# Kernel optimization log

Hardware: AMD Instinct MI355X
Metric: run time of the kernel (lower is better)

Reference implementation:

```python
import jax, jax.numpy as jnp
import numpy as np


def _conv1x1(x, W, b):
    # x: [B, Cin, H, W]; W: [Cout, Cin]; b: [Cout] -- 1x1 conv == channel matmul
    return jnp.einsum('oc,bchw->bohw', W, x) + b[None, :, None, None]


def setup_inputs() -> dict:
    key = jax.random.key(0)
    ks = jax.random.split(key, 9)
    B, C, H, W = 8, 64, 64, 64
    x = jax.random.normal(ks[0], (B, C, H, W), dtype=jnp.float32)
    y = jax.random.normal(ks[1], (B, C, H, W), dtype=jnp.float32)
    scale = 1.0 / np.sqrt(C)
    Wq = jax.random.normal(ks[2], (C, C), dtype=jnp.float32) * scale
    bq = jax.random.normal(ks[3], (C,), dtype=jnp.float32) * 0.01
    Wk = jax.random.normal(ks[4], (C, C), dtype=jnp.float32) * scale
    bk = jax.random.normal(ks[5], (C,), dtype=jnp.float32) * 0.01
    Wv = jax.random.normal(ks[6], (C, C), dtype=jnp.float32) * scale
    bv = jax.random.normal(ks[7], (C,), dtype=jnp.float32) * 0.01
    # torch inits gamma to 0; use small nonzero value so output/grads are non-trivial
    gamma = jax.random.normal(ks[8], (1,), dtype=jnp.float32) * 0.1
    return {"x": x, "y": y, "Wq": Wq, "bq": bq, "Wk": Wk, "bk": bk,
            "Wv": Wv, "bv": bv, "gamma": gamma}


def reference(x, y, Wq, bq, Wk, bk, Wv, bv, gamma):
    B, C, H, W = x.shape
    N = H * W
    q = _conv1x1(x, Wq, bq)  # [B, C, H, W]
    k = _conv1x1(y, Wk, bk)
    v = _conv1x1(y, Wv, bv)
    # Faithful to torch: raw .view(B, -1, C) memory reinterpretation (NOT a transpose)
    qf = q.reshape(B, N, C)   # reinterprets [B,C,H,W] buffer as [B, N, C]
    kf = k.reshape(B, C, N)
    vf = v.reshape(B, C, N)
    att = jnp.einsum('bnc,bcm->bnm', qf, kf)          # [B, N, N], unscaled
    att = jax.nn.softmax(att, axis=-1)
    out = jnp.einsum('bcj,bij->bci', vf, att)         # bmm(v, att^T) -> [B, C, N]
    out = out.reshape(B, C, H, W)
    return gamma[0] * out + x
```

## Files before the change

### kernel.cpp

```cpp
#include <hip/hip_runtime.h>
#include <math.h>

#define Bb 8
#define Cc 64
#define Nn 4096

typedef __attribute__((ext_vector_type(8))) short bf16x8;
typedef __attribute__((ext_vector_type(4))) float f32x4;
typedef __attribute__((ext_vector_type(4))) int   i32x4;

#define MFMA(a,b,c) __builtin_amdgcn_mfma_f32_16x16x32_bf16((a),(b),(c),0,0,0)

__device__ __forceinline__ unsigned short f2bf(float f){
    unsigned uu = __float_as_uint(f);
    return (unsigned short)((uu + 0x7FFFu + ((uu>>16)&1u)) >> 16);
}
__device__ __forceinline__ int swzaddr(int row, int slot){
    int h = (row ^ (row>>3)) & 7;
    return row*128 + (((slot ^ h)&7)<<4);
}

#define YT0   0
#define YTT0  8192
#define P0    16384

__global__ __launch_bounds__(512, 2) void fused_attn_mfma(
    const float* __restrict__ x, const float* __restrict__ y,
    const float* __restrict__ Wq, const float* __restrict__ bq,
    const float* __restrict__ Wk, const float* __restrict__ bk,
    const float* __restrict__ Wv, const float* __restrict__ bv,
    const float* __restrict__ gammap, float* __restrict__ out)
{
    __shared__ __align__(16) float QbL[2*4096];
    __shared__ __align__(16) unsigned char RBp[32768];
    __shared__ float qbsL[128];
    __shared__ float WqL[128];
    __shared__ float bqL[2];
    __shared__ float bkL[64];

    const int tid = threadIdx.x;
    const int l   = tid & 63;
    const int w   = tid >> 6;
    const int l15 = l & 15;
    const int u   = l >> 4;
    const int b   = blockIdx.x >> 5;
    const int pb  = blockIdx.x & 31;
    const int c0  = pb*2;
    const int p0  = pb*128;

    const float* __restrict__ xb = x + (size_t)b*Cc*Nn;
    const float* __restrict__ yb = y + (size_t)b*Cc*Nn;

    if (tid < 128) WqL[tid] = Wq[c0*64 + tid];
    if (tid < 2)   bqL[tid] = bq[c0 + tid];
    if (tid < 64)  bkL[tid] = bk[tid];
    {
        float* WkL = (float*)RBp;
        #pragma unroll
        for (int q2 = 0; q2 < 2; ++q2){
            const int idx = tid*8 + q2*4;
            *(float4*)(&WkL[idx]) = *(const float4*)(Wk + idx);
        }
    }
    __syncthreads();

    {
        const int pp = tid*8;
        float q0[8], q1[8];
        const float bq0 = bqL[0], bq1 = bqL[1];
        #pragma unroll
        for (int k2=0;k2<8;++k2){ q0[k2]=bq0; q1[k2]=bq1; }
        #pragma unroll 4
        for (int cx=0; cx<64; ++cx){
            const float wa = WqL[cx], wb = WqL[64+cx];
            const float4 x0 = *(const float4*)(xb + cx*Nn + pp);
            const float4 x1 = *(const float4*)(xb + cx*Nn + pp + 4);
            q0[0]=fmaf(wa,x0.x,q0[0]); q0[1]=fmaf(wa,x0.y,q0[1]);
            q0[2]=fmaf(wa,x0.z,q0[2]); q0[3]=fmaf(wa,x0.w,q0[3]);
            q0[4]=fmaf(wa,x1.x,q0[4]); q0[5]=fmaf(wa,x1.y,q0[5]);
            q0[6]=fmaf(wa,x1.z,q0[6]); q0[7]=fmaf(wa,x1.w,q0[7]);
            q1[0]=fmaf(wb,x0.x,q1[0]); q1[1]=fmaf(wb,x0.y,q1[1]);
            q1[2]=fmaf(wb,x0.z,q1[2]); q1[3]=fmaf(wb,x0.w,q1[3]);
            q1[4]=fmaf(wb,x1.x,q1[4]); q1[5]=fmaf(wb,x1.y,q1[5]);
            q1[6]=fmaf(wb,x1.z,q1[6]); q1[7]=fmaf(wb,x1.w,q1[7]);
        }
        *(float4*)(&QbL[pp])        = make_float4(q0[0],q0[1],q0[2],q0[3]);
        *(float4*)(&QbL[pp+4])      = make_float4(q0[4],q0[5],q0[6],q0[7]);
        *(float4*)(&QbL[4096+pp])   = make_float4(q1[0],q1[1],q1[2],q1[3]);
        *(float4*)(&QbL[4096+pp+4]) = make_float4(q1[4],q1[5],q1[6],q1[7]);
    }
    __syncthreads();

    if (tid < 128) {
        const float* qr = &QbL[(tid>>6)*4096 + (tid&63)*64];
        float a = 0.f;
        #pragma unroll 8
        for (int c=0;c<64;++c) a = fmaf(qr[c], bkL[c], a);
        qbsL[tid] = a;
    }
    f32x4 D2[4];
    {
        const float* WkL = (const float*)RBp;
        bf16x8 wkA[4][2];
        #pragma unroll
        for (int mb=0; mb<4; ++mb){
            const int ci = mb*16 + l15;
            #pragma unroll
            for (int kc=0; kc<2; ++kc){
                bf16x8 t;
                #pragma unroll
                for (int i=0;i<8;++i) t[i] = (short)f2bf(WkL[(kc*32 + u*8 + i)*64 + ci]);
                wkA[mb][kc] = t;
            }
        }
        bf16x8 qbB[2];
        {
            const int t = w*16 + l15;
            const float* qr = &QbL[(t>>6)*4096 + (t&63)*64];
            #pragma unroll
            for (int kc=0; kc<2; ++kc){
                const float4 f0 = *(const float4*)(qr + kc*32 + u*8);
                const float4 f1 = *(const float4*)(qr + kc*32 + u*8 + 4);
                bf16x8 t;
                t[0]=(short)f2bf(f0.x); t[1]=(short)f2bf(f0.y);
                t[2]=(short)f2bf(f0.z); t[3]=(short)f2bf(f0.w);
                t[4]=(short)f2bf(f1.x); t[5]=(short)f2bf(f1.y);
                t[6]=(short)f2bf(f1.z); t[7]=(short)f2bf(f1.w);
                qbB[kc] = t;
            }
        }
        #pragma unroll
        for (int mb=0;mb<4;++mb){
            f32x4 d = {0.f,0.f,0.f,0.f};
            d = MFMA(wkA[mb][0], qbB[0], d);
            d = MFMA(wkA[mb][1], qbB[1], d);
            D2[mb] = d;
        }
    }
    __syncthreads();

    unsigned char* QWp = (unsigned char*)QbL;
    {
        const int t = w*16 + l15;
        #pragma unroll
        for (int mb=0;mb<4;++mb){
            #pragma unroll
            for (int r=0;r<4;++r){
                const int ci = mb*16 + u*4 + r;
                *(unsigned short*)(QWp + swzaddr(t, ci>>3) + (ci&7)*2) = f2bf(D2[mb][r]);
            }
        }
    }
    bf16x8 qwA0, qwA1;
    {
        const int t = w*16 + l15;
        qwA0 = *(const bf16x8*)(QWp + swzaddr(t, u));
        qwA1 = *(const bf16x8*)(QWp + swzaddr(t, 4 + u));
    }
    float qb4[4];
    #pragma unroll
    for (int r=0;r<4;++r) qb4[r] = qbsL[w*16 + u*4 + r];

    const int sci = tid >> 3;
    const int sjj = (tid & 7) * 8;
    int rA[4][2], paA[2], pwA2[4][4], trA[8];
    #pragma unroll
    for (int nb=0;nb<4;++nb){
        const int row = 16*nb + l15;
        rA[nb][0] = swzaddr(row, u);
        rA[nb][1] = swzaddr(row, 4 + u);
    }
    paA[0] = P0 + swzaddr(w*16 + l15, u);
    paA[1] = P0 + swzaddr(w*16 + l15, 4 + u);
    #pragma unroll
    for (int r=0;r<4;++r){
        const int trow = w*16 + u*4 + r;
        #pragma unroll
        for (int nb=0;nb<4;++nb)
            pwA2[r][nb] = P0 + swzaddr(trow, (l15>>3) + 2*nb) + (l&7)*2;
    }
    const int natA = YT0 + swzaddr(sci, tid & 7);
    #pragma unroll
    for (int k=0;k<8;++k)
        trA[k] = YTT0 + swzaddr(sjj + k, sci>>3) + (sci&7)*2;

    f32x4 PY[4];
    #pragma unroll
    for (int nb=0;nb<4;++nb) PY[nb] = (f32x4){0.f,0.f,0.f,0.f};
    float m4[4], l4[4];
    #pragma unroll
    for (int r=0;r<4;++r){ m4[r] = -1.0e30f; l4[r] = 0.f; }

    const float* ybt = yb + sci*Nn + sjj;
    float4 ra0 = *(const float4*)(ybt);
    float4 ra1 = *(const float4*)(ybt + 4);
    float4 rb0, rb1;

    auto tile_body = [&](int jt, float4& A0, float4& A1, float4& N0, float4& N1) {
        unsigned short e0=f2bf(A0.x), e1=f2bf(A0.y), e2=f2bf(A0.z), e3=f2bf(A0.w);
        unsigned short e4=f2bf(A1.x), e5=f2bf(A1.y), e6=f2bf(A1.z), e7=f2bf(A1.w);
        i32x4 pk;
        pk.x = (int)e0 | ((int)e1<<16);
        pk.y = (int)e2 | ((int)e3<<16);
        pk.z = (int)e4 | ((int)e5<<16);
        pk.w = (int)e6 | ((int)e7<<16);
        *(i32x4*)(RBp + natA) = pk;
        *(unsigned short*)(RBp + trA[0]) = e0;
        *(unsigned short*)(RBp + trA[1]) = e1;
        *(unsigned short*)(RBp + trA[2]) = e2;
        *(unsigned short*)(RBp + trA[3]) = e3;
        *(unsigned short*)(RBp + trA[4]) = e4;
        *(unsigned short*)(RBp + trA[5]) = e5;
        *(unsigned short*)(RBp + trA[6]) = e6;
        *(unsigned short*)(RBp + trA[7]) = e7;
        __syncthreads();
        {
            const float* yn = ybt + ((jt+1)&63)*64;
            N0 = *(const float4*)(yn);
            N1 = *(const float4*)(yn + 4);
        }
        f32x4 S[4];
        #pragma unroll
        for (int nb=0;nb<4;++nb){
            f32x4 s = (f32x4){qb4[0],qb4[1],qb4[2],qb4[3]};
            s = MFMA(qwA0, *(const bf16x8*)(RBp + YTT0 + rA[nb][0]), s);
            s = MFMA(qwA1, *(const bf16x8*)(RBp + YTT0 + rA[nb][1]), s);
            S[nb] = s;
        }
        float pm[4];
        #pragma unroll
        for (int r=0;r<4;++r)
            pm[r] = fmaxf(fmaxf(S[0][r],S[1][r]), fmaxf(S[2][r],S[3][r]));
        #pragma unroll
        for (int st=1; st<16; st<<=1){
            #pragma unroll
            for (int r=0;r<4;++r) pm[r] = fmaxf(pm[r], __shfl_xor(pm[r], st));
        }
        float sc[4], rs[4];
        #pragma unroll
        for (int r=0;r<4;++r){
            const float mn = fmaxf(m4[r], pm[r]);
            sc[r] = __expf(m4[r] - mn);
            m4[r] = mn;
            rs[r] = 0.f;
        }
        #pragma unroll
        for (int nb=0;nb<4;++nb){
            #pragma unroll
            for (int r=0;r<4;++r){
                const float e = __expf(S[nb][r] - m4[r]);
                S[nb][r] = e;
                rs[r] += e;
            }
        }
        #pragma unroll
        for (int st=1; st<16; st<<=1){
            #pragma unroll
            for (int r=0;r<4;++r) rs[r] += __shfl_xor(rs[r], st);
        }
        #pragma unroll
        for (int r=0;r<4;++r) l4[r] = l4[r]*sc[r] + rs[r];
        #pragma unroll
        for (int nb=0;nb<4;++nb){
            #pragma unroll
            for (int r=0;r<4;++r) PY[nb][r] *= sc[r];
        }
        #pragma unroll
        for (int r=0;r<4;++r){
            #pragma unroll
            for (int nb=0;nb<4;++nb)
                *(unsigned short*)(RBp + pwA2[r][nb]) = f2bf(S[nb][r]);
        }
        bf16x8 pa0 = *(const bf16x8*)(RBp + paA[0]);
        bf16x8 pa1 = *(const bf16x8*)(RBp + paA[1]);
        #pragma unroll
        for (int nb=0;nb<4;++nb){
            f32x4 acc = PY[nb];
            acc = MFMA(pa0, *(const bf16x8*)(RBp + YT0 + rA[nb][0]), acc);
            acc = MFMA(pa1, *(const bf16x8*)(RBp + YT0 + rA[nb][1]), acc);
            PY[nb] = acc;
        }
        __syncthreads();
    };

    for (int jt = 0; jt < 64; jt += 2) {
        tile_body(jt,   ra0, ra1, rb0, rb1);
        tile_body(jt+1, rb0, rb1, ra0, ra1);
    }

    float inv[4];
    #pragma unroll
    for (int r=0;r<4;++r) inv[r] = 1.0f / l4[r];
    #pragma unroll
    for (int r=0;r<4;++r){
        #pragma unroll
        for (int nb=0;nb<4;++nb)
            *(unsigned short*)(RBp + pwA2[r][nb]) = f2bf(PY[nb][r] * inv[r]);
    }
    __syncthreads();

    {
        const int mc = (w & 3) * 16;
        const int tbase = (w >> 2) * 64;
        bf16x8 wvA[2];
        #pragma unroll
        for (int kc=0; kc<2; ++kc){
            const float* wr = Wv + (mc + l15)*64 + kc*32 + u*8;
            const float4 f0 = *(const float4*)(wr);
            const float4 f1 = *(const float4*)(wr + 4);
            bf16x8 t;
            t[0]=(short)f2bf(f0.x); t[1]=(short)f2bf(f0.y);
            t[2]=(short)f2bf(f0.z); t[3]=(short)f2bf(f0.w);
            t[4]=(short)f2bf(f1.x); t[5]=(short)f2bf(f1.y);
            t[6]=(short)f2bf(f1.z); t[7]=(short)f2bf(f1.w);
            wvA[kc] = t;
        }
        f32x4 O[4];
        #pragma unroll
        for (int nb2=0; nb2<4; ++nb2){
            f32x4 o = (f32x4){0.f,0.f,0.f,0.f};
            const int trow = tbase + nb2*16 + l15;
            o = MFMA(wvA[0], *(const bf16x8*)(RBp + P0 + swzaddr(trow, u)), o);
            o = MFMA(wvA[1], *(const bf16x8*)(RBp + P0 + swzaddr(trow, 4 + u)), o);
            O[nb2] = o;
        }
        const float g = gammap[0];
        #pragma unroll
        for (int r=0;r<4;++r){
            const int c = mc + u*4 + r;
            const float bvc = bv[c];
            #pragma unroll
            for (int nb2=0; nb2<4; ++nb2){
                const int t = tbase + nb2*16 + l15;
                const size_t oi = (size_t)b*Cc*Nn + (size_t)c*Nn + p0 + t;
                out[oi] = g*(O[nb2][r] + bvc) + x[oi];
            }
        }
    }
}

extern "C" void kernel_launch(void* const* d_in, const int* in_sizes, int n_in,
                              void* d_out, int out_size, void* d_ws, size_t ws_size,
                              hipStream_t stream) {
    const float* x  = (const float*)d_in[0];
    const float* y  = (const float*)d_in[1];
    const float* Wq = (const float*)d_in[2];
    const float* bq = (const float*)d_in[3];
    const float* Wk = (const float*)d_in[4];
    const float* bk = (const float*)d_in[5];
    const float* Wv = (const float*)d_in[6];
    const float* bv = (const float*)d_in[7];
    const float* g  = (const float*)d_in[8];
    float* outp = (float*)d_out;
    dim3 grid(Bb * 32), block(512);
    hipLaunchKernelGGL(fused_attn_mfma, grid, block, 0, stream,
                       x, y, Wq, bq, Wk, bk, Wv, bv, g, outp);
}
```

Baseline: 224.3 us.

## Split Q projection into separate MFMA kernel and restructure attention with double-buffered tiles

Moves the Q 1x1-conv into its own kernel that uses split-bf16 (hi/lo) MFMA and writes bf16 Q to workspace. The attention kernel now uses 256-thread blocks over 64-row tiles, giving a grid of 512 blocks. It double-buffers the y tiles in LDS and drops the bk bias term, which is constant per row and cancels in the softmax. It also switches to exp2 with log2e folded into Q·Wk and defers rescaling of the running max unless the max grows past a threshold. These changes aim to raise parallelism, cut the per-block serial Q compute and the exp cost, at the price of an extra launch and a workspace round-trip.

```diff
diff --git a/kernel.cpp b/kernel.cpp
--- a/kernel.cpp
+++ b/kernel.cpp
@@ -4,6 +4,8 @@
 #define Bb 8
 #define Cc 64
 #define Nn 4096
+#define LOG2E 1.4426950408889634f
+#define DEFER_TH 8.0f
 
 typedef __attribute__((ext_vector_type(8))) short bf16x8;
 typedef __attribute__((ext_vector_type(4))) float f32x4;
@@ -11,178 +13,230 @@
 
 #define MFMA(a,b,c) __builtin_amdgcn_mfma_f32_16x16x32_bf16((a),(b),(c),0,0,0)
 
+#if __has_builtin(__builtin_amdgcn_exp2f)
+#define EXP2F(x) __builtin_amdgcn_exp2f(x)
+#else
+#define EXP2F(x) exp2f(x)
+#endif
+
 __device__ __forceinline__ unsigned short f2bf(float f){
     unsigned uu = __float_as_uint(f);
     return (unsigned short)((uu + 0x7FFFu + ((uu>>16)&1u)) >> 16);
 }
+__device__ __forceinline__ float bfres(float f, unsigned short h){
+    return f - __uint_as_float(((unsigned)h)<<16);
+}
 __device__ __forceinline__ int swzaddr(int row, int slot){
     int h = (row ^ (row>>3)) & 7;
     return row*128 + (((slot ^ h)&7)<<4);
 }
 
-#define YT0   0
-#define YTT0  8192
-#define P0    16384
-
-__global__ __launch_bounds__(512, 2) void fused_attn_mfma(
-    const float* __restrict__ x, const float* __restrict__ y,
-    const float* __restrict__ Wq, const float* __restrict__ bq,
-    const float* __restrict__ Wk, const float* __restrict__ bk,
-    const float* __restrict__ Wv, const float* __restrict__ bv,
-    const float* __restrict__ gammap, float* __restrict__ out)
+__global__ __launch_bounds__(256) void precompute_q(
+    const float* __restrict__ x, const float* __restrict__ Wq,
+    const float* __restrict__ bq, unsigned short* __restrict__ wsq)
 {
-    __shared__ __align__(16) float QbL[2*4096];
-    __shared__ __align__(16) unsigned char RBp[32768];
-    __shared__ float qbsL[128];
-    __shared__ float WqL[128];
-    __shared__ float bqL[2];
-    __shared__ float bkL[64];
-
+    __shared__ __align__(16) unsigned char XHI[16384];
+    __shared__ __align__(16) unsigned char XLO[16384];
     const int tid = threadIdx.x;
     const int l   = tid & 63;
     const int w   = tid >> 6;
     const int l15 = l & 15;
     const int u   = l >> 4;
-    const int b   = blockIdx.x >> 5;
-    const int pb  = blockIdx.x & 31;
-    const int c0  = pb*2;
-    const int p0  = pb*128;
-
-    const float* __restrict__ xb = x + (size_t)b*Cc*Nn;
+    const int b   = blockIdx.x & 7;
+    const int pt  = blockIdx.x >> 3;
+    const int p0  = pt*128;
+
+    bf16x8 whiA[2], wloA[2];
+    #pragma unroll
+    for (int kc=0; kc<2; ++kc){
+        const float* wr = Wq + (16*w + l15)*64 + kc*32 + u*8;
+        const float4 f0 = *(const float4*)(wr);
+        const float4 f1 = *(const float4*)(wr + 4);
+        const float vv[8] = {f0.x,f0.y,f0.z,f0.w,f1.x,f1.y,f1.z,f1.w};
+        bf16x8 hi, lo;
+        #pragma unroll
+        for (int i=0;i<8;++i){
+            const unsigned short h = f2bf(vv[i]);
+            hi[i] = (short)h;
+            lo[i] = (short)f2bf(bfres(vv[i], h));
+        }
+        whiA[kc]=hi; wloA[kc]=lo;
+    }
+    {
+        const int cx0 = (tid & 31)*2;
+        const int pq  = (tid >> 5)*16;
+        const float* xr0 = x + ((size_t)b*64 + cx0)*4096 + p0 + pq;
+        const float* xr1 = xr0 + 4096;
+        #pragma unroll
+        for (int q4=0; q4<4; ++q4){
+            const float4 a = *(const float4*)(xr0 + q4*4);
+            const float4 c = *(const float4*)(xr1 + q4*4);
+            const float av[4]={a.x,a.y,a.z,a.w}, cv[4]={c.x,c.y,c.z,c.w};
+            #pragma unroll
+            for (int k=0;k<4;++k){
+                const int p = pq + q4*4 + k;
+                const unsigned short h0=f2bf(av[k]), h1=f2bf(cv[k]);
+                const unsigned short l0=f2bf(bfres(av[k],h0));
+                const unsigned short l1=f2bf(bfres(cv[k],h1));
+                const int ad = swzaddr(p, cx0>>3) + (cx0&7)*2;
+                *(unsigned int*)(XHI + ad) = (unsigned)h0 | ((unsigned)h1<<16);
+                *(unsigned int*)(XLO + ad) = (unsigned)l0 | ((unsigned)l1<<16);
+            }
+        }
+    }
+    __syncthreads();
+
+    f32x4 D[8];
+    #pragma unroll
+    for (int nb=0;nb<8;++nb) D[nb]=(f32x4){0.f,0.f,0.f,0.f};
+    #pragma unroll
+    for (int nb=0;nb<8;++nb){
+        #pragma unroll
+        for (int kc=0;kc<2;++kc){
+            const int ad = swzaddr(16*nb + l15, kc*4 + u);
+            const bf16x8 xh = *(const bf16x8*)(XHI + ad);
+            const bf16x8 xl = *(const bf16x8*)(XLO + ad);
+            D[nb] = MFMA(whiA[kc], xh, D[nb]);
+            D[nb] = MFMA(whiA[kc], xl, D[nb]);
+            D[nb] = MFMA(wloA[kc], xh, D[nb]);
+        }
+    }
+    float bq4[4];
+    #pragma unroll
+    for (int r=0;r<4;++r) bq4[r] = bq[16*w + u*4 + r];
+    #pragma unroll
+    for (int nb=0;nb<8;++nb){
+        #pragma unroll
+        for (int r=0;r<4;++r){
+            const int c = 16*w + u*4 + r;
+            const int p = p0 + 16*nb + l15;
+            wsq[((size_t)b*64 + c)*4096 + p] = f2bf(D[nb][r] + bq4[r]);
+        }
+    }
+}
+
+__global__ __launch_bounds__(256,2) void fused_attn2(
+    const float* __restrict__ x, const float* __restrict__ y,
+    const float* __restrict__ Wk, const unsigned short* __restrict__ wsq,
+    const float* __restrict__ Wv, const float* __restrict__ bv,
+    const float* __restrict__ gammap, float* __restrict__ out)
+{
+    __shared__ __align__(16) unsigned char QW [8192];
+    __shared__ __align__(16) unsigned char PT [8192];
+    __shared__ __align__(16) unsigned char WKT[8192];
+    __shared__ __align__(16) unsigned char YN [2][8192];
+    __shared__ __align__(16) unsigned char YT [2][8192];
+
+    const int tid = threadIdx.x;
+    const int l   = tid & 63;
+    const int w   = tid >> 6;
+    const int l15 = l & 15;
+    const int u   = l >> 4;
+    const int b   = blockIdx.x & 7;
+    const int blk = blockIdx.x >> 3;
+    const int p0  = blk*64;
+
     const float* __restrict__ yb = y + (size_t)b*Cc*Nn;
 
-    if (tid < 128) WqL[tid] = Wq[c0*64 + tid];
-    if (tid < 2)   bqL[tid] = bq[c0 + tid];
-    if (tid < 64)  bkL[tid] = bk[tid];
-    {
-        float* WkL = (float*)RBp;
-        #pragma unroll
-        for (int q2 = 0; q2 < 2; ++q2){
-            const int idx = tid*8 + q2*4;
-            *(float4*)(&WkL[idx]) = *(const float4*)(Wk + idx);
-        }
+    const int sci = tid >> 2;
+    const int sj0 = (tid & 3) * 16;
+
+    float4 pf0, pf1, pf2, pf3;
+    {
+        const float* yr = yb + (size_t)sci*Nn + sj0;
+        pf0 = *(const float4*)(yr);
+        pf1 = *(const float4*)(yr + 4);
+        pf2 = *(const float4*)(yr + 8);
+        pf3 = *(const float4*)(yr + 12);
+    }
+
+    {
+        const int c   = tid >> 2;
+        const int ci0 = (tid & 3)*16;
+        const float* wr = Wk + c*64 + ci0;
+        #pragma unroll
+        for (int q4=0; q4<4; ++q4){
+            const float4 f = *(const float4*)(wr + q4*4);
+            const float fv[4] = {f.x,f.y,f.z,f.w};
+            #pragma unroll
+            for (int k=0;k<4;++k){
+                const int ci = ci0 + q4*4 + k;
+                *(unsigned short*)(WKT + swzaddr(ci, c>>3) + (c&7)*2) = f2bf(fv[k]);
+            }
+        }
+    }
+    bf16x8 qA[2];
+    {
+        const unsigned short* qchan = wsq + ((size_t)b*64 + blk)*4096;
+        #pragma unroll
+        for (int kc=0;kc<2;++kc)
+            qA[kc] = *(const bf16x8*)(qchan + 64*(16*w + l15) + kc*32 + u*8);
     }
     __syncthreads();
 
     {
-        const int pp = tid*8;
-        float q0[8], q1[8];
-        const float bq0 = bqL[0], bq1 = bqL[1];
-        #pragma unroll
-        for (int k2=0;k2<8;++k2){ q0[k2]=bq0; q1[k2]=bq1; }
-        #pragma unroll 4
-        for (int cx=0; cx<64; ++cx){
-            const float wa = WqL[cx], wb = WqL[64+cx];
-            const float4 x0 = *(const float4*)(xb + cx*Nn + pp);
-            const float4 x1 = *(const float4*)(xb + cx*Nn + pp + 4);
-            q0[0]=fmaf(wa,x0.x,q0[0]); q0[1]=fmaf(wa,x0.y,q0[1]);
-            q0[2]=fmaf(wa,x0.z,q0[2]); q0[3]=fmaf(wa,x0.w,q0[3]);
-            q0[4]=fmaf(wa,x1.x,q0[4]); q0[5]=fmaf(wa,x1.y,q0[5]);
-            q0[6]=fmaf(wa,x1.z,q0[6]); q0[7]=fmaf(wa,x1.w,q0[7]);
-            q1[0]=fmaf(wb,x0.x,q1[0]); q1[1]=fmaf(wb,x0.y,q1[1]);
-            q1[2]=fmaf(wb,x0.z,q1[2]); q1[3]=fmaf(wb,x0.w,q1[3]);
-            q1[4]=fmaf(wb,x1.x,q1[4]); q1[5]=fmaf(wb,x1.y,q1[5]);
-            q1[6]=fmaf(wb,x1.z,q1[6]); q1[7]=fmaf(wb,x1.w,q1[7]);
-        }
-        *(float4*)(&QbL[pp])        = make_float4(q0[0],q0[1],q0[2],q0[3]);
-        *(float4*)(&QbL[pp+4])      = make_float4(q0[4],q0[5],q0[6],q0[7]);
-        *(float4*)(&QbL[4096+pp])   = make_float4(q1[0],q1[1],q1[2],q1[3]);
-        *(float4*)(&QbL[4096+pp+4]) = make_float4(q1[4],q1[5],q1[6],q1[7]);
-    }
+        f32x4 D2[4];
+        #pragma unroll
+        for (int nb=0;nb<4;++nb){
+            f32x4 d = (f32x4){0.f,0.f,0.f,0.f};
+            d = MFMA(qA[0], *(const bf16x8*)(WKT + swzaddr(16*nb + l15, u)),     d);
+            d = MFMA(qA[1], *(const bf16x8*)(WKT + swzaddr(16*nb + l15, 4 + u)), d);
+            D2[nb] = d;
+        }
+        #pragma unroll
+        for (int nb=0;nb<4;++nb){
+            #pragma unroll
+            for (int r=0;r<4;++r){
+                const int t  = 16*w + u*4 + r;
+                const int ci = 16*nb + l15;
+                *(unsigned short*)(QW + swzaddr(t, 2*nb + (l15>>3)) + (l15&7)*2)
+                    = f2bf(D2[nb][r] * LOG2E);
+            }
+        }
+    }
+    bf16x8 qwA[2];
+    qwA[0] = *(const bf16x8*)(QW + swzaddr(16*w + l15, u));
+    qwA[1] = *(const bf16x8*)(QW + swzaddr(16*w + l15, 4 + u));
+
+    int rd[4][2];
+    #pragma unroll
+    for (int nb=0;nb<4;++nb){
+        rd[nb][0] = swzaddr(16*nb + l15, u);
+        rd[nb][1] = swzaddr(16*nb + l15, 4 + u);
+    }
+    const int paA0 = swzaddr(16*w + l15, u);
+    const int paA1 = swzaddr(16*w + l15, 4 + u);
+    int pw[4][4];
+    #pragma unroll
+    for (int r=0;r<4;++r)
+        #pragma unroll
+        for (int nb=0;nb<4;++nb)
+            pw[r][nb] = swzaddr(16*w + u*4 + r, 2*nb + (l15>>3)) + (l15&7)*2;
+
+    auto stage_write = [&](float4 a0, float4 a1, float4 a2, float4 a3, int buf){
+        const float v[16] = {a0.x,a0.y,a0.z,a0.w, a1.x,a1.y,a1.z,a1.w,
+                             a2.x,a2.y,a2.z,a2.w, a3.x,a3.y,a3.z,a3.w};
+        unsigned short e[16];
+        #pragma unroll
+        for (int k=0;k<16;++k) e[k] = f2bf(v[k]);
+        i32x4 pk0, pk1;
+        pk0.x = (int)((unsigned)e[0]  | ((unsigned)e[1]<<16));
+        pk0.y = (int)((unsigned)e[2]  | ((unsigned)e[3]<<16));
+        pk0.z = (int)((unsigned)e[4]  | ((unsigned)e[5]<<16));
+        pk0.w = (int)((unsigned)e[6]  | ((unsigned)e[7]<<16));
+        pk1.x = (int)((unsigned)e[8]  | ((unsigned)e[9]<<16));
+        pk1.y = (int)((unsigned)e[10] | ((unsigned)e[11]<<16));
+        pk1.z = (int)((unsigned)e[12] | ((unsigned)e[13]<<16));
+        pk1.w = (int)((unsigned)e[14] | ((unsigned)e[15]<<16));
+        *(i32x4*)(YN[buf] + swzaddr(sci, (sj0>>3)))     = pk0;
+        *(i32x4*)(YN[buf] + swzaddr(sci, (sj0>>3) + 1)) = pk1;
+        #pragma unroll
+        for (int k=0;k<16;++k)
+            *(unsigned short*)(YT[buf] + swzaddr(sj0 + k, sci>>3) + (sci&7)*2) = e[k];
+    };
+
+    stage_write(pf0, pf1, pf2, pf3, 0);
     __syncthreads();
-
-    if (tid < 128) {
-        const float* qr = &QbL[(tid>>6)*4096 + (tid&63)*64];
-        float a = 0.f;
-        #pragma unroll 8
-        for (int c=0;c<64;++c) a = fmaf(qr[c], bkL[c], a);
-        qbsL[tid] = a;
-    }
-    f32x4 D2[4];
-    {
-        const float* WkL = (const float*)RBp;
-        bf16x8 wkA[4][2];
-        #pragma unroll
-        for (int mb=0; mb<4; ++mb){
-            const int ci = mb*16 + l15;
-            #pragma unroll
-            for (int kc=0; kc<2; ++kc){
-                bf16x8 t;
-                #pragma unroll
-                for (int i=0;i<8;++i) t[i] = (short)f2bf(WkL[(kc*32 + u*8 + i)*64 + ci]);
-                wkA[mb][kc] = t;
-            }
-        }
-        bf16x8 qbB[2];
-        {
-            const int t = w*16 + l15;
-            const float* qr = &QbL[(t>>6)*4096 + (t&63)*64];
-            #pragma unroll
-            for (int kc=0; kc<2; ++kc){
-                const float4 f0 = *(const float4*)(qr + kc*32 + u*8);
-                const float4 f1 = *(const float4*)(qr + kc*32 + u*8 + 4);
-                bf16x8 t;
-                t[0]=(short)f2bf(f0.x); t[1]=(short)f2bf(f0.y);
-                t[2]=(short)f2bf(f0.z); t[3]=(short)f2bf(f0.w);
-                t[4]=(short)f2bf(f1.x); t[5]=(short)f2bf(f1.y);
-                t[6]=(short)f2bf(f1.z); t[7]=(short)f2bf(f1.w);
-                qbB[kc] = t;
-            }
-        }
-        #pragma unroll
-        for (int mb=0;mb<4;++mb){
-            f32x4 d = {0.f,0.f,0.f,0.f};
-            d = MFMA(wkA[mb][0], qbB[0], d);
-            d = MFMA(wkA[mb][1], qbB[1], d);
-            D2[mb] = d;
-        }
-    }
-    __syncthreads();
-
-    unsigned char* QWp = (unsigned char*)QbL;
-    {
-        const int t = w*16 + l15;
-        #pragma unroll
-        for (int mb=0;mb<4;++mb){
-            #pragma unroll
-            for (int r=0;r<4;++r){
-                const int ci = mb*16 + u*4 + r;
-                *(unsigned short*)(QWp + swzaddr(t, ci>>3) + (ci&7)*2) = f2bf(D2[mb][r]);
-            }
-        }
-    }
-    bf16x8 qwA0, qwA1;
-    {
-        const int t = w*16 + l15;
-        qwA0 = *(const bf16x8*)(QWp + swzaddr(t, u));
-        qwA1 = *(const bf16x8*)(QWp + swzaddr(t, 4 + u));
-    }
-    float qb4[4];
-    #pragma unroll
-    for (int r=0;r<4;++r) qb4[r] = qbsL[w*16 + u*4 + r];
-
-    const int sci = tid >> 3;
-    const int sjj = (tid & 7) * 8;
-    int rA[4][2], paA[2], pwA2[4][4], trA[8];
-    #pragma unroll
-    for (int nb=0;nb<4;++nb){
-        const int row = 16*nb + l15;
-        rA[nb][0] = swzaddr(row, u);
-        rA[nb][1] = swzaddr(row, 4 + u);
-    }
-    paA[0] = P0 + swzaddr(w*16 + l15, u);
-    paA[1] = P0 + swzaddr(w*16 + l15, 4 + u);
-    #pragma unroll
-    for (int r=0;r<4;++r){
-        const int trow = w*16 + u*4 + r;
-        #pragma unroll
-        for (int nb=0;nb<4;++nb)
-            pwA2[r][nb] = P0 + swzaddr(trow, (l15>>3) + 2*nb) + (l&7)*2;
-    }
-    const int natA = YT0 + swzaddr(sci, tid & 7);
-    #pragma unroll
-    for (int k=0;k<8;++k)
-        trA[k] = YTT0 + swzaddr(sjj + k, sci>>3) + (sci&7)*2;
 
     f32x4 PY[4];
     #pragma unroll
@@ -191,40 +245,22 @@
     #pragma unroll
     for (int r=0;r<4;++r){ m4[r] = -1.0e30f; l4[r] = 0.f; }
 
-    const float* ybt = yb + sci*Nn + sjj;
-    float4 ra0 = *(const float4*)(ybt);
-    float4 ra1 = *(const float4*)(ybt + 4);
-    float4 rb0, rb1;
-
-    auto tile_body = [&](int jt, float4& A0, float4& A1, float4& N0, float4& N1) {
-        unsigned short e0=f2bf(A0.x), e1=f2bf(A0.y), e2=f2bf(A0.z), e3=f2bf(A0.w);
-        unsigned short e4=f2bf(A1.x), e5=f2bf(A1.y), e6=f2bf(A1.z), e7=f2bf(A1.w);
-        i32x4 pk;
-        pk.x = (int)e0 | ((int)e1<<16);
-        pk.y = (int)e2 | ((int)e3<<16);
-        pk.z = (int)e4 | ((int)e5<<16);
-        pk.w = (int)e6 | ((int)e7<<16);
-        *(i32x4*)(RBp + natA) = pk;
-        *(unsigned short*)(RBp + trA[0]) = e0;
-        *(unsigned short*)(RBp + trA[1]) = e1;
-        *(unsigned short*)(RBp + trA[2]) = e2;
-        *(unsigned short*)(RBp + trA[3]) = e3;
-        *(unsigned short*)(RBp + trA[4]) = e4;
-        *(unsigned short*)(RBp + trA[5]) = e5;
-        *(unsigned short*)(RBp + trA[6]) = e6;
-        *(unsigned short*)(RBp + trA[7]) = e7;
-        __syncthreads();
-        {
-            const float* yn = ybt + ((jt+1)&63)*64;
-            N0 = *(const float4*)(yn);
-            N1 = *(const float4*)(yn + 4);
+    for (int jt = 0; jt < 64; ++jt){
+        const int cur = jt & 1;
+        float4 n0,n1,n2,n3;
+        if (jt < 63){
+            const float* yr = yb + (size_t)sci*Nn + (jt+1)*64 + sj0;
+            n0 = *(const float4*)(yr);
+            n1 = *(const float4*)(yr + 4);
+            n2 = *(const float4*)(yr + 8);
+            n3 = *(const float4*)(yr + 12);
         }
         f32x4 S[4];
         #pragma unroll
         for (int nb=0;nb<4;++nb){
-            f32x4 s = (f32x4){qb4[0],qb4[1],qb4[2],qb4[3]};
-            s = MFMA(qwA0, *(const bf16x8*)(RBp + YTT0 + rA[nb][0]), s);
-            s = MFMA(qwA1, *(const bf16x8*)(RBp + YTT0 + rA[nb][1]), s);
+            f32x4 s = (f32x4){0.f,0.f,0.f,0.f};
+            s = MFMA(qwA[0], *(const bf16x8*)(YT[cur] + rd[nb][0]), s);
+            s = MFMA(qwA[1], *(const bf16x8*)(YT[cur] + rd[nb][1]), s);
             S[nb] = s;
         }
         float pm[4];
@@ -236,19 +272,26 @@
             #pragma unroll
             for (int r=0;r<4;++r) pm[r] = fmaxf(pm[r], __shfl_xor(pm[r], st));
         }
-        float sc[4], rs[4];
-        #pragma unroll
-        for (int r=0;r<4;++r){
-            const float mn = fmaxf(m4[r], pm[r]);
-            sc[r] = __expf(m4[r] - mn);
-            m4[r] = mn;
-            rs[r] = 0.f;
-        }
-        #pragma unroll
-        for (int nb=0;nb<4;++nb){
+        bool need = false;
+        #pragma unroll
+        for (int r=0;r<4;++r) need = need || (pm[r] > m4[r] + DEFER_TH);
+        if (__ballot(need)) {
             #pragma unroll
             for (int r=0;r<4;++r){
-                const float e = __expf(S[nb][r] - m4[r]);
+                const float mn = fmaxf(m4[r], pm[r]);
+                const float sc = EXP2F(m4[r] - mn);
+                m4[r] = mn;
+                l4[r] *= sc;
+                #pragma unroll
+                for (int nb=0;nb<4;++nb) PY[nb][r] *= sc;
+            }
+        }
+        float rs[4] = {0.f,0.f,0.f,0.f};
+        #pragma unroll
+        for (int nb=0;nb<4;++nb){
+            #pragma unroll
+            for (int r=0;r<4;++r){
+                const float e = EXP2F(S[nb][r] - m4[r]);
                 S[nb][r] = e;
                 rs[r] += e;
             }
@@ -259,81 +302,69 @@
             for (int r=0;r<4;++r) rs[r] += __shfl_xor(rs[r], st);
         }
         #pragma unroll
-        for (int r=0;r<4;++r) l4[r] = l4[r]*sc[r] + rs[r];
-        #pragma unroll
-        for (int nb=0;nb<4;++nb){
-            #pragma unroll
-            for (int r=0;r<4;++r) PY[nb][r] *= sc[r];
-        }
-        #pragma unroll
-        for (int r=0;r<4;++r){
+        for (int r=0;r<4;++r) l4[r] += rs[r];
+
+        #pragma unroll
+        for (int r=0;r<4;++r)
             #pragma unroll
             for (int nb=0;nb<4;++nb)
-                *(unsigned short*)(RBp + pwA2[r][nb]) = f2bf(S[nb][r]);
-        }
-        bf16x8 pa0 = *(const bf16x8*)(RBp + paA[0]);
-        bf16x8 pa1 = *(const bf16x8*)(RBp + paA[1]);
-        #pragma unroll
-        for (int nb=0;nb<4;++nb){
-            f32x4 acc = PY[nb];
-            acc = MFMA(pa0, *(const bf16x8*)(RBp + YT0 + rA[nb][0]), acc);
-            acc = MFMA(pa1, *(const bf16x8*)(RBp + YT0 + rA[nb][1]), acc);
-            PY[nb] = acc;
-        }
+                *(unsigned short*)(PT + pw[r][nb]) = f2bf(S[nb][r]);
+        {
+            const bf16x8 pa0 = *(const bf16x8*)(PT + paA0);
+            const bf16x8 pa1 = *(const bf16x8*)(PT + paA1);
+            #pragma unroll
+            for (int nb=0;nb<4;++nb){
+                f32x4 acc = PY[nb];
+                acc = MFMA(pa0, *(const bf16x8*)(YN[cur] + rd[nb][0]), acc);
+                acc = MFMA(pa1, *(const bf16x8*)(YN[cur] + rd[nb][1]), acc);
+                PY[nb] = acc;
+            }
+        }
+        if (jt < 63) stage_write(n0, n1, n2, n3, cur ^ 1);
         __syncthreads();
-    };
-
-    for (int jt = 0; jt < 64; jt += 2) {
-        tile_body(jt,   ra0, ra1, rb0, rb1);
-        tile_body(jt+1, rb0, rb1, ra0, ra1);
     }
 
     float inv[4];
     #pragma unroll
     for (int r=0;r<4;++r) inv[r] = 1.0f / l4[r];
     #pragma unroll
-    for (int r=0;r<4;++r){
+    for (int r=0;r<4;++r)
         #pragma unroll
         for (int nb=0;nb<4;++nb)
-            *(unsigned short*)(RBp + pwA2[r][nb]) = f2bf(PY[nb][r] * inv[r]);
-    }
+            *(unsigned short*)(PT + pw[r][nb]) = f2bf(PY[nb][r] * inv[r]);
     __syncthreads();
 
     {
-        const int mc = (w & 3) * 16;
-        const int tbase = (w >> 2) * 64;
         bf16x8 wvA[2];
         #pragma unroll
-        for (int kc=0; kc<2; ++kc){
-            const float* wr = Wv + (mc + l15)*64 + kc*32 + u*8;
+        for (int kc=0;kc<2;++kc){
+            const float* wr = Wv + (16*w + l15)*64 + kc*32 + u*8;
             const float4 f0 = *(const float4*)(wr);
             const float4 f1 = *(const float4*)(wr + 4);
+            const float vv[8] = {f0.x,f0.y,f0.z,f0.w,f1.x,f1.y,f1.z,f1.w};
             bf16x8 t;
-            t[0]=(short)f2bf(f0.x); t[1]=(short)f2bf(f0.y);
-            t[2]=(short)f2bf(f0.z); t[3]=(short)f2bf(f0.w);
-            t[4]=(short)f2bf(f1.x); t[5]=(short)f2bf(f1.y);
-            t[6]=(short)f2bf(f1.z); t[7]=(short)f2bf(f1.w);
+            #pragma unroll
+            for (int i=0;i<8;++i) t[i] = (short)f2bf(vv[i]);
             wvA[kc] = t;
         }
         f32x4 O[4];
         #pragma unroll
-        for (int nb2=0; nb2<4; ++nb2){
+        for (int nb=0;nb<4;++nb){
             f32x4 o = (f32x4){0.f,0.f,0.f,0.f};
-            const int trow = tbase + nb2*16 + l15;
-            o = MFMA(wvA[0], *(const bf16x8*)(RBp + P0 + swzaddr(trow, u)), o);
-            o = MFMA(wvA[1], *(const bf16x8*)(RBp + P0 + swzaddr(trow, 4 + u)), o);
-            O[nb2] = o;
+            o = MFMA(wvA[0], *(const bf16x8*)(PT + rd[nb][0]), o);
+            o = MFMA(wvA[1], *(const bf16x8*)(PT + rd[nb][1]), o);
+            O[nb] = o;
         }
         const float g = gammap[0];
         #pragma unroll
         for (int r=0;r<4;++r){
-            const int c = mc + u*4 + r;
-            const float bvc = bv[c];
-            #pragma unroll
-            for (int nb2=0; nb2<4; ++nb2){
-                const int t = tbase + nb2*16 + l15;
-                const size_t oi = (size_t)b*Cc*Nn + (size_t)c*Nn + p0 + t;
-                out[oi] = g*(O[nb2][r] + bvc) + x[oi];
+            const int cout = 16*w + u*4 + r;
+            const float bvc = bv[cout];
+            #pragma unroll
+            for (int nb=0;nb<4;++nb){
+                const int t = 16*nb + l15;
+                const size_t oi = ((size_t)b*64 + cout)*4096 + p0 + t;
+                out[oi] = g*(O[nb][r] + bvc) + x[oi];
             }
         }
     }
@@ -347,12 +378,14 @@
     const float* Wq = (const float*)d_in[2];
     const float* bq = (const float*)d_in[3];
     const float* Wk = (const float*)d_in[4];
-    const float* bk = (const float*)d_in[5];
     const float* Wv = (const float*)d_in[6];
     const float* bv = (const float*)d_in[7];
     const float* g  = (const float*)d_in[8];
     float* outp = (float*)d_out;
-    dim3 grid(Bb * 32), block(512);
-    hipLaunchKernelGGL(fused_attn_mfma, grid, block, 0, stream,
-                       x, y, Wq, bq, Wk, bk, Wv, bv, g, outp);
-}
+    unsigned short* wsq = (unsigned short*)d_ws;
+
+    hipLaunchKernelGGL(precompute_q, dim3(256), dim3(256), 0, stream,
+                       x, Wq, bq, wsq);
+    hipLaunchKernelGGL(fused_attn2, dim3(512), dim3(256), 0, stream,
+                       x, y, Wk, wsq, Wv, bv, g, outp);
+}
```

New measurement: 221.2 us. No clear change (-1.4%).
